# Kernel optimization log

Measured on AMD Instinct MI355X. Metric: run time of the kernel, lower is better.

## Reference

```python
import jax, jax.numpy as jnp
import numpy as np

N = 50000      # nodes
E = 800000     # edges (avg degree 16)
D = 128        # in_dim
H = 128        # hidden_dim
C = 10         # num_classes
G = 128        # graphs in batch
NUM_LAYERS = 3


def setup_inputs() -> dict:
    key = jax.random.key(0)
    ks = jax.random.split(key, 32)
    inp = {
        'features': jax.random.normal(ks[0], (N, D), dtype=jnp.float32),
        'src': jax.random.randint(ks[1], (E,), 0, N, dtype=jnp.int32),
        'dst': jax.random.randint(ks[2], (E,), 0, N, dtype=jnp.int32),
        'graph_ids': jnp.sort(jax.random.randint(ks[3], (N,), 0, G, dtype=jnp.int32)),
        'eps': jnp.zeros((NUM_LAYERS,), dtype=jnp.float32),  # learn_eps=True, init 0
    }
    # GIN MLPs: layer i has linear1 [in,H], linear2 [H,H] (stored as [in,out])
    ki = 4
    for i in range(NUM_LAYERS):
        din = D if i == 0 else H
        inp[f'w1_{i}'] = jax.random.normal(ks[ki], (din, H), dtype=jnp.float32) * (1.0 / np.sqrt(din)); ki += 1
        inp[f'b1_{i}'] = jnp.zeros((H,), dtype=jnp.float32)
        inp[f'w2_{i}'] = jax.random.normal(ks[ki], (H, H), dtype=jnp.float32) * (1.0 / np.sqrt(H)); ki += 1
        inp[f'b2_{i}'] = jnp.zeros((H,), dtype=jnp.float32)
    inp['wc1'] = jax.random.normal(ks[ki], (H, H), dtype=jnp.float32) * (1.0 / np.sqrt(H)); ki += 1
    inp['bc1'] = jnp.zeros((H,), dtype=jnp.float32)
    inp['wc2'] = jax.random.normal(ks[ki], (H, C), dtype=jnp.float32) * (1.0 / np.sqrt(H)); ki += 1
    inp['bc2'] = jnp.zeros((C,), dtype=jnp.float32)
    return inp


def _mlp(x, w1, b1, w2, b2):
    return jax.nn.relu(x @ w1 + b1) @ w2 + b2


def reference(features, src, dst, graph_ids, eps,
              w1_0, b1_0, w2_0, b2_0,
              w1_1, b1_1, w2_1, b2_1,
              w1_2, b1_2, w2_2, b2_2,
              wc1, bc1, wc2, bc2):
    mlps = [(w1_0, b1_0, w2_0, b2_0), (w1_1, b1_1, w2_1, b2_1), (w1_2, b1_2, w2_2, b2_2)]
    h = features
    for i, (w1, b1, w2, b2) in enumerate(mlps):
        # GINConv: aggregate sum of in-neighbor features (gather src, segment-sum into dst)
        agg = jax.ops.segment_sum(h[src], dst, num_segments=N)
        h = (1.0 + eps[i]) * h + agg
        h = _mlp(h, w1, b1, w2, b2)
        h = jax.nn.relu(h)
    # SumPooling: nodes -> graphs
    hg = jax.ops.segment_sum(h, graph_ids, num_segments=G)  # [G, H]
    out = jax.nn.relu(hg @ wc1 + bc1) @ wc2 + bc2            # [G, C]
    return out
```

## Files before the change

### kernel.cpp

```cpp
#include <hip/hip_runtime.h>

#define NN 50000
#define EE 800000
#define HH 128
#define CC 10
#define GG 128
#define NBK 782
#define NCH 98
#define CHUNK 8192

typedef __attribute__((ext_vector_type(8))) short short8;
typedef __attribute__((ext_vector_type(4))) float f32x4;

__device__ __forceinline__ ushort f2b(float f) {
    union { float f; uint u; } x; x.f = f;
    uint u = x.u;
    uint r = (u + 0x7fffu + ((u >> 16) & 1u)) >> 16;
    return (ushort)r;
}
__device__ __forceinline__ float lo2f(uint v) {
    union { uint u; float f; } x; x.u = v << 16; return x.f;
}
__device__ __forceinline__ float hi2f(uint v) {
    union { uint u; float f; } x; x.u = v & 0xffff0000u; return x.f;
}


__global__ __launch_bounds__(256) void hist_kernel(const int* __restrict__ dst,
                                                   int* __restrict__ hist) {
    __shared__ int hc[NBK];
    const int c = blockIdx.x, t = threadIdx.x;
    for (int k = t; k < NBK; k += 256) hc[k] = 0;
    __syncthreads();
    for (int j = 0; j < 32; ++j) {
        int e = c * CHUNK + j * 256 + t;
        if (e < EE) atomicAdd(&hc[dst[e] >> 6], 1);
    }
    __syncthreads();
    for (int k = t; k < NBK; k += 256) hist[k * NCH + c] = hc[k];
}

__global__ __launch_bounds__(128) void bscan_kernel(const int* __restrict__ hist,
                                                    int* __restrict__ rel,
                                                    int* __restrict__ btot) {
    __shared__ int s[128];
    const int b = blockIdx.x, t = threadIdx.x;
    int v = (t < NCH) ? hist[b * NCH + t] : 0;
    s[t] = v;
    __syncthreads();
    for (int off = 1; off < 128; off <<= 1) {
        int tt = (t >= off) ? s[t - off] : 0;
        __syncthreads();
        s[t] += tt;
        __syncthreads();
    }
    if (t < NCH) rel[b * NCH + t] = s[t] - v;
    if (t == 127) btot[b] = s[127];
}

__global__ __launch_bounds__(1024) void tscan_kernel(const int* __restrict__ btot,
                                                     int* __restrict__ bucketptr,
                                                     int* __restrict__ rowptr) {
    __shared__ int s[1024];
    const int t = threadIdx.x;
    int v = (t < NBK) ? btot[t] : 0;
    s[t] = v;
    __syncthreads();
    for (int off = 1; off < 1024; off <<= 1) {
        int tt = (t >= off) ? s[t - off] : 0;
        __syncthreads();
        s[t] += tt;
        __syncthreads();
    }
    if (t < NBK) bucketptr[t] = s[t] - v;
    if (t == 0) { bucketptr[NBK] = EE; rowptr[NN] = EE; }
}

__global__ __launch_bounds__(256) void scatter_kernel(const int* __restrict__ src,
                                                      const int* __restrict__ dst,
                                                      const int* __restrict__ rel,
                                                      const int* __restrict__ bucketptr,
                                                      int* __restrict__ epk) {
    __shared__ int cur[NBK];
    const int c = blockIdx.x, t = threadIdx.x;
    for (int k = t; k < NBK; k += 256) cur[k] = bucketptr[k] + rel[k * NCH + c];
    __syncthreads();
    for (int j = 0; j < 32; ++j) {
        int e = c * CHUNK + j * 256 + t;
        if (e < EE) {
            int d = dst[e];
            int bk = d >> 6;
            int pos = atomicAdd(&cur[bk], 1);
            epk[pos] = ((d & 63) << 16) | src[e];
        }
    }
}

__global__ __launch_bounds__(256) void bsort_kernel(const int* __restrict__ epk,
                                                    const int* __restrict__ bucketptr,
                                                    int* __restrict__ eidx,
                                                    int* __restrict__ rowptr) {
    __shared__ int cnt[64];
    __shared__ int cur[64];
    const int b = blockIdx.x, t = threadIdx.x;
    const int base = bucketptr[b], end = bucketptr[b + 1];
    if (t < 64) cnt[t] = 0;
    __syncthreads();
    for (int i = base + t; i < end; i += 256)
        atomicAdd(&cnt[(epk[i] >> 16) & 63], 1);
    __syncthreads();
    if (t < 64) {
        int v = cnt[t];
        int incl = v;
#pragma unroll
        for (int off = 1; off < 64; off <<= 1) {
            int u = __shfl_up(incl, off);
            if (t >= off) incl += u;
        }
        int excl = incl - v;
        cur[t] = excl;
        int node = b * 64 + t;
        if (node < NN) rowptr[node] = base + excl;
    }
    __syncthreads();
    for (int i = base + t; i < end; i += 256) {
        int p = epk[i];
        int dl = (p >> 16) & 63;
        int pos = atomicAdd(&cur[dl], 1);
        eidx[base + pos] = p & 0xffff;
    }
}


__global__ __launch_bounds__(256) void f2b_kernel(const float* __restrict__ in,
                                                  ushort* __restrict__ out, int n4) {
    int i = blockIdx.x * 256 + threadIdx.x;
    if (i < n4) {
        float4 v = ((const float4*)in)[i];
        ushort4 o;
        o.x = f2b(v.x); o.y = f2b(v.y); o.z = f2b(v.z); o.w = f2b(v.w);
        ((ushort4*)out)[i] = o;
    }
}

__global__ __launch_bounds__(256) void wconv_kernel(const float* w0, const float* w1,
                                                    const float* w2, const float* w3,
                                                    const float* w4, const float* w5,
                                                    ushort* __restrict__ wt) {
    const float* src;
    switch (blockIdx.y) {
        case 0: src = w0; break; case 1: src = w1; break;
        case 2: src = w2; break; case 3: src = w3; break;
        case 4: src = w4; break; default: src = w5; break;
    }
    int idx = blockIdx.x * 256 + threadIdx.x;
    int n = idx >> 7, k = idx & 127;
    wt[blockIdx.y * 16384 + n * 128 + k] = f2b(src[k * 128 + n]);
}


__global__ __launch_bounds__(256) void aggregate_kernel(const ushort* __restrict__ h,
                                                        const int* __restrict__ rowptr,
                                                        const int* __restrict__ eidx,
                                                        ushort* __restrict__ agg) {
    int node = blockIdx.x * 4 + (threadIdx.x >> 6);
    if (node >= NN) return;
    int lane = threadIdx.x & 63;
    int beg = rowptr[node], end = rowptr[node + 1];
    float ax = 0.f, ay = 0.f;
    int i = beg;
    for (; i + 8 <= end; i += 8) {
        uint v[8];
#pragma unroll
        for (int k = 0; k < 8; ++k) {
            int s = eidx[i + k];
            v[k] = *(const uint*)(h + (size_t)s * HH + lane * 2);
        }
#pragma unroll
        for (int k = 0; k < 8; ++k) { ax += lo2f(v[k]); ay += hi2f(v[k]); }
    }
    for (; i < end; ++i) {
        int s = eidx[i];
        uint v = *(const uint*)(h + (size_t)s * HH + lane * 2);
        ax += lo2f(v); ay += hi2f(v);
    }
    uint o = (uint)f2b(ax) | (((uint)f2b(ay)) << 16);
    *(uint*)(agg + (size_t)node * HH + lane * 2) = o;
}


__device__ __forceinline__ uint comb2(uint hv, uint av, float e) {
    float fl = e * lo2f(hv) + lo2f(av);
    float fh = e * hi2f(hv) + hi2f(av);
    return (uint)f2b(fl) | (((uint)f2b(fh)) << 16);
}

__global__ __launch_bounds__(256) void fused_mlp(const ushort* __restrict__ xin,
                                                 const ushort* __restrict__ agg,
                                                 const ushort* __restrict__ wt1,
                                                 const ushort* __restrict__ wt2,
                                                 const float* __restrict__ b1,
                                                 const float* __restrict__ b2,
                                                 const float* __restrict__ epsp, int layer,
                                                 ushort* __restrict__ out, int nrows) {
    __shared__ __align__(16) ushort xs[64][136];
    __shared__ __align__(16) ushort hs[64][136];
    const int tid = threadIdx.x;
    const int lane = tid & 63, w = tid >> 6;
    const int row0 = blockIdx.x * 64;
    const int l15 = lane & 15, lhi = lane >> 4;

    short8 a1[2][4], a2[2][4];
#pragma unroll
    for (int fa = 0; fa < 2; ++fa)
#pragma unroll
        for (int kt = 0; kt < 4; ++kt) {
            int n = w * 32 + fa * 16 + l15;
            int k = kt * 32 + lhi * 8;
            a1[fa][kt] = *(const short8*)(wt1 + n * HH + k);
            a2[fa][kt] = *(const short8*)(wt2 + n * HH + k);
        }

    float eps1 = 1.0f + epsp[layer];
#pragma unroll
    for (int it = 0; it < 4; ++it) {
        int idx = it * 256 + tid;
        int r = idx >> 4, kq = idx & 15;
        int row = row0 + r;
        uint4 xv = make_uint4(0u, 0u, 0u, 0u);
        if (row < nrows) {
            xv = *(const uint4*)(xin + (size_t)row * HH + kq * 8);
            uint4 av = *(const uint4*)(agg + (size_t)row * HH + kq * 8);
            xv.x = comb2(xv.x, av.x, eps1);
            xv.y = comb2(xv.y, av.y, eps1);
            xv.z = comb2(xv.z, av.z, eps1);
            xv.w = comb2(xv.w, av.w, eps1);
        }
        *(uint4*)&xs[r][kq * 8] = xv;
    }
    __syncthreads();

    f32x4 acc[2][4];
#pragma unroll
    for (int fa = 0; fa < 2; ++fa)
#pragma unroll
        for (int fb = 0; fb < 4; ++fb) acc[fa][fb] = (f32x4)(0.f);
#pragma unroll
    for (int kt = 0; kt < 4; ++kt) {
        short8 bfr[4];
#pragma unroll
        for (int fb = 0; fb < 4; ++fb)
            bfr[fb] = *(const short8*)&xs[fb * 16 + l15][kt * 32 + lhi * 8];
#pragma unroll
        for (int fa = 0; fa < 2; ++fa)
#pragma unroll
            for (int fb = 0; fb < 4; ++fb)
                acc[fa][fb] = __builtin_amdgcn_mfma_f32_16x16x32_bf16(a1[fa][kt], bfr[fb],
                                                                     acc[fa][fb], 0, 0, 0);
    }

#pragma unroll
    for (int fa = 0; fa < 2; ++fa) {
        int nb = w * 32 + fa * 16 + lhi * 4;
        float4 bv = *(const float4*)(b1 + nb);
#pragma unroll
        for (int fb = 0; fb < 4; ++fb) {
            ushort4 o;
            o.x = f2b(fmaxf(acc[fa][fb][0] + bv.x, 0.f));
            o.y = f2b(fmaxf(acc[fa][fb][1] + bv.y, 0.f));
            o.z = f2b(fmaxf(acc[fa][fb][2] + bv.z, 0.f));
            o.w = f2b(fmaxf(acc[fa][fb][3] + bv.w, 0.f));
            *(ushort4*)&hs[fb * 16 + l15][nb] = o;
        }
    }
    __syncthreads();

#pragma unroll
    for (int fa = 0; fa < 2; ++fa)
#pragma unroll
        for (int fb = 0; fb < 4; ++fb) acc[fa][fb] = (f32x4)(0.f);
#pragma unroll
    for (int kt = 0; kt < 4; ++kt) {
        short8 bfr[4];
#pragma unroll
        for (int fb = 0; fb < 4; ++fb)
            bfr[fb] = *(const short8*)&hs[fb * 16 + l15][kt * 32 + lhi * 8];
#pragma unroll
        for (int fa = 0; fa < 2; ++fa)
#pragma unroll
            for (int fb = 0; fb < 4; ++fb)
                acc[fa][fb] = __builtin_amdgcn_mfma_f32_16x16x32_bf16(a2[fa][kt], bfr[fb],
                                                                     acc[fa][fb], 0, 0, 0);
    }

#pragma unroll
    for (int fa = 0; fa < 2; ++fa) {
        int nb = w * 32 + fa * 16 + lhi * 4;
        float4 bv = *(const float4*)(b2 + nb);
#pragma unroll
        for (int fb = 0; fb < 4; ++fb) {
            int m = row0 + fb * 16 + l15;
            if (m < nrows) {
                ushort4 o;
                o.x = f2b(fmaxf(acc[fa][fb][0] + bv.x, 0.f));
                o.y = f2b(fmaxf(acc[fa][fb][1] + bv.y, 0.f));
                o.z = f2b(fmaxf(acc[fa][fb][2] + bv.z, 0.f));
                o.w = f2b(fmaxf(acc[fa][fb][3] + bv.w, 0.f));
                *(ushort4*)(out + (size_t)m * HH + nb) = o;
            }
        }
    }
}


__global__ __launch_bounds__(256) void pool_kernel(const ushort* __restrict__ h,
                                                   const int* __restrict__ gid,
                                                   float* hg) {
    int j = threadIdx.x & 63;
    int r0 = threadIdx.x >> 6;
    int n0 = blockIdx.x * 64;
    float ax = 0.f, ay = 0.f;
    int gcur = -1;
#pragma unroll
    for (int i = 0; i < 16; ++i) {
        int n = n0 + r0 + i * 4;
        if (n >= NN) break;
        int g = gid[n];
        if (g != gcur) {
            if (gcur >= 0) {
                atomicAdd(&hg[gcur * HH + 2 * j], ax);
                atomicAdd(&hg[gcur * HH + 2 * j + 1], ay);
            }
            gcur = g; ax = 0.f; ay = 0.f;
        }
        uint v = *(const uint*)(h + (size_t)n * HH + 2 * j);
        ax += lo2f(v); ay += hi2f(v);
    }
    if (gcur >= 0) {
        atomicAdd(&hg[gcur * HH + 2 * j], ax);
        atomicAdd(&hg[gcur * HH + 2 * j + 1], ay);
    }
}


__global__ __launch_bounds__(128) void classify_kernel(const float* __restrict__ hg,
                                                       const float* __restrict__ wc1,
                                                       const float* __restrict__ bc1,
                                                       const float* __restrict__ wc2,
                                                       const float* __restrict__ bc2,
                                                       float* __restrict__ out) {
    __shared__ float xrow[HH];
    __shared__ float trow[HH];
    int g = blockIdx.x, j = threadIdx.x;
    xrow[j] = hg[g * HH + j];
    __syncthreads();
    float s = bc1[j];
#pragma unroll 8
    for (int k = 0; k < HH; ++k) s += xrow[k] * wc1[k * HH + j];
    trow[j] = fmaxf(s, 0.f);
    __syncthreads();
    if (j < CC) {
        float o = bc2[j];
#pragma unroll 8
        for (int k = 0; k < HH; ++k) o += trow[k] * wc2[k * CC + j];
        out[g * CC + j] = o;
    }
}

extern "C" void kernel_launch(void* const* d_in, const int* in_sizes, int n_in,
                              void* d_out, int out_size, void* d_ws, size_t ws_size,
                              hipStream_t stream) {
    const float* features = (const float*)d_in[0];
    const int* src = (const int*)d_in[1];
    const int* dst = (const int*)d_in[2];
    const int* gid = (const int*)d_in[3];
    const float* eps = (const float*)d_in[4];
    const float* w1[3] = {(const float*)d_in[5], (const float*)d_in[9], (const float*)d_in[13]};
    const float* b1[3] = {(const float*)d_in[6], (const float*)d_in[10], (const float*)d_in[14]};
    const float* w2[3] = {(const float*)d_in[7], (const float*)d_in[11], (const float*)d_in[15]};
    const float* b2[3] = {(const float*)d_in[8], (const float*)d_in[12], (const float*)d_in[16]};
    const float* wc1 = (const float*)d_in[17];
    const float* bc1 = (const float*)d_in[18];
    const float* wc2 = (const float*)d_in[19];
    const float* bc2 = (const float*)d_in[20];
    float* outp = (float*)d_out;

    char* ws = (char*)d_ws;
    size_t off = 0;
    auto alloc = [&](size_t bytes) {
        void* p = ws + off;
        off += (bytes + 255) & ~(size_t)255;
        return p;
    };
    int* hist = (int*)alloc((size_t)NBK * NCH * sizeof(int));
    int* rel = (int*)alloc((size_t)NBK * NCH * sizeof(int));
    int* btot = (int*)alloc(NBK * sizeof(int));
    int* bucketptr = (int*)alloc((NBK + 1) * sizeof(int));
    int* epk = (int*)alloc(EE * sizeof(int));
    int* eidx = (int*)alloc(EE * sizeof(int));
    int* rowptr = (int*)alloc((NN + 1) * sizeof(int));
    ushort* hb0 = (ushort*)alloc((size_t)NN * HH * 2);
    ushort* hb1 = (ushort*)alloc((size_t)NN * HH * 2);
    ushort* hb2 = (ushort*)alloc((size_t)NN * HH * 2);
    ushort* aggb = (ushort*)alloc((size_t)NN * HH * 2);
    ushort* wtb = (ushort*)alloc(6 * 16384 * 2);
    float* hg = (float*)alloc(GG * HH * sizeof(float));

    hist_kernel<<<NCH, 256, 0, stream>>>(dst, hist);
    bscan_kernel<<<NBK, 128, 0, stream>>>(hist, rel, btot);
    tscan_kernel<<<1, 1024, 0, stream>>>(btot, bucketptr, rowptr);
    scatter_kernel<<<NCH, 256, 0, stream>>>(src, dst, rel, bucketptr, epk);
    bsort_kernel<<<NBK, 256, 0, stream>>>(epk, bucketptr, eidx, rowptr);

    f2b_kernel<<<(NN * HH / 4 + 255) / 256, 256, 0, stream>>>(features, hb0, NN * HH / 4);
    dim3 wg(64, 6);
    wconv_kernel<<<wg, 256, 0, stream>>>(w1[0], w2[0], w1[1], w2[1], w1[2], w2[2], wtb);

    const int GB = (NN + 63) / 64;

    const ushort* hin = hb0;
    ushort* houts[3] = {hb1, hb2, hb1};
    for (int i = 0; i < 3; ++i) {
        aggregate_kernel<<<(NN + 3) / 4, 256, 0, stream>>>(hin, rowptr, eidx, aggb);
        fused_mlp<<<GB, 256, 0, stream>>>(hin, aggb, wtb + (2 * i) * 16384,
                                          wtb + (2 * i + 1) * 16384,
                                          b1[i], b2[i], eps, i, houts[i], NN);
        hin = houts[i];
    }

    hipMemsetAsync(hg, 0, GG * HH * sizeof(float), stream);
    pool_kernel<<<(NN + 63) / 64, 256, 0, stream>>>(hb1, gid, hg);
    classify_kernel<<<GG, 128, 0, stream>>>(hg, wc1, bc1, wc2, bc2, outp);
}
```

Measured before the change: 246.8 us.

## Fuse eps-combine into aggregation, pooling into last MLP, split-edge gather

The aggregation kernel now has each wave split into two half-waves that process alternating edges with 8-byte loads, reduces the halves with a lane shuffle, and writes (1+eps)*h + agg directly. The MLP therefore reads one input tensor instead of two. The final layer's MLP writes its output into shared memory and does the graph sum-pooling with atomics, so the last hidden tensor is never written to global memory and the separate pool kernel is removed. The risks are lower memory-level parallelism per lane in the gather, and extra sync and atomic work added to the tail of the last MLP.

After: 233.3 us. 5.5% less time.

```diff
diff --git a/kernel.cpp b/kernel.cpp
--- a/kernel.cpp
+++ b/kernel.cpp
@@ -162,46 +162,58 @@
 __global__ __launch_bounds__(256) void aggregate_kernel(const ushort* __restrict__ h,
                                                         const int* __restrict__ rowptr,
                                                         const int* __restrict__ eidx,
-                                                        ushort* __restrict__ agg) {
+                                                        const float* __restrict__ epsp,
+                                                        int layer,
+                                                        ushort* __restrict__ xb) {
     int node = blockIdx.x * 4 + (threadIdx.x >> 6);
     if (node >= NN) return;
     int lane = threadIdx.x & 63;
+    int half = lane >> 5, li = lane & 31;
     int beg = rowptr[node], end = rowptr[node + 1];
-    float ax = 0.f, ay = 0.f;
-    int i = beg;
-    for (; i + 8 <= end; i += 8) {
-        uint v[8];
-#pragma unroll
-        for (int k = 0; k < 8; ++k) {
-            int s = eidx[i + k];
-            v[k] = *(const uint*)(h + (size_t)s * HH + lane * 2);
-        }
-#pragma unroll
-        for (int k = 0; k < 8; ++k) { ax += lo2f(v[k]); ay += hi2f(v[k]); }
-    }
-    for (; i < end; ++i) {
-        int s = eidx[i];
-        uint v = *(const uint*)(h + (size_t)s * HH + lane * 2);
-        ax += lo2f(v); ay += hi2f(v);
-    }
-    uint o = (uint)f2b(ax) | (((uint)f2b(ay)) << 16);
-    *(uint*)(agg + (size_t)node * HH + lane * 2) = o;
-}
-
-
-__device__ __forceinline__ uint comb2(uint hv, uint av, float e) {
-    float fl = e * lo2f(hv) + lo2f(av);
-    float fh = e * hi2f(hv) + hi2f(av);
-    return (uint)f2b(fl) | (((uint)f2b(fh)) << 16);
-}
-
-__global__ __launch_bounds__(256) void fused_mlp(const ushort* __restrict__ xin,
-                                                 const ushort* __restrict__ agg,
+    float c0 = 0.f, c1 = 0.f, c2 = 0.f, c3 = 0.f;
+    int i = beg + half;
+    for (; i + 6 < end; i += 8) {
+        int s0 = eidx[i], s1 = eidx[i + 2], s2 = eidx[i + 4], s3 = eidx[i + 6];
+        uint2 v0 = *(const uint2*)(h + (size_t)s0 * HH + li * 4);
+        uint2 v1 = *(const uint2*)(h + (size_t)s1 * HH + li * 4);
+        uint2 v2 = *(const uint2*)(h + (size_t)s2 * HH + li * 4);
+        uint2 v3 = *(const uint2*)(h + (size_t)s3 * HH + li * 4);
+        c0 += lo2f(v0.x) + lo2f(v1.x) + lo2f(v2.x) + lo2f(v3.x);
+        c1 += hi2f(v0.x) + hi2f(v1.x) + hi2f(v2.x) + hi2f(v3.x);
+        c2 += lo2f(v0.y) + lo2f(v1.y) + lo2f(v2.y) + lo2f(v3.y);
+        c3 += hi2f(v0.y) + hi2f(v1.y) + hi2f(v2.y) + hi2f(v3.y);
+    }
+    for (; i < end; i += 2) {
+        int s0 = eidx[i];
+        uint2 v0 = *(const uint2*)(h + (size_t)s0 * HH + li * 4);
+        c0 += lo2f(v0.x); c1 += hi2f(v0.x);
+        c2 += lo2f(v0.y); c3 += hi2f(v0.y);
+    }
+    c0 += __shfl_xor(c0, 32);
+    c1 += __shfl_xor(c1, 32);
+    c2 += __shfl_xor(c2, 32);
+    c3 += __shfl_xor(c3, 32);
+    if (half == 0) {
+        uint2 hv = *(const uint2*)(h + (size_t)node * HH + li * 4);
+        float e = 1.0f + epsp[layer];
+        ushort4 o;
+        o.x = f2b(e * lo2f(hv.x) + c0);
+        o.y = f2b(e * hi2f(hv.x) + c1);
+        o.z = f2b(e * lo2f(hv.y) + c2);
+        o.w = f2b(e * hi2f(hv.y) + c3);
+        *(ushort4*)(xb + (size_t)node * HH + li * 4) = o;
+    }
+}
+
+
+template <bool LAST>
+__global__ __launch_bounds__(256) void fused_mlp(const ushort* __restrict__ xb,
                                                  const ushort* __restrict__ wt1,
                                                  const ushort* __restrict__ wt2,
                                                  const float* __restrict__ b1,
                                                  const float* __restrict__ b2,
-                                                 const float* __restrict__ epsp, int layer,
+                                                 const int* __restrict__ gid,
+                                                 float* __restrict__ hg,
                                                  ushort* __restrict__ out, int nrows) {
     __shared__ __align__(16) ushort xs[64][136];
     __shared__ __align__(16) ushort hs[64][136];
@@ -221,21 +233,13 @@
             a2[fa][kt] = *(const short8*)(wt2 + n * HH + k);
         }
 
-    float eps1 = 1.0f + epsp[layer];
 #pragma unroll
     for (int it = 0; it < 4; ++it) {
         int idx = it * 256 + tid;
         int r = idx >> 4, kq = idx & 15;
         int row = row0 + r;
         uint4 xv = make_uint4(0u, 0u, 0u, 0u);
-        if (row < nrows) {
-            xv = *(const uint4*)(xin + (size_t)row * HH + kq * 8);
-            uint4 av = *(const uint4*)(agg + (size_t)row * HH + kq * 8);
-            xv.x = comb2(xv.x, av.x, eps1);
-            xv.y = comb2(xv.y, av.y, eps1);
-            xv.z = comb2(xv.z, av.z, eps1);
-            xv.w = comb2(xv.w, av.w, eps1);
-        }
+        if (row < nrows) xv = *(const uint4*)(xb + (size_t)row * HH + kq * 8);
         *(uint4*)&xs[r][kq * 8] = xv;
     }
     __syncthreads();
@@ -300,45 +304,45 @@
 #pragma unroll
         for (int fb = 0; fb < 4; ++fb) {
             int m = row0 + fb * 16 + l15;
-            if (m < nrows) {
-                ushort4 o;
-                o.x = f2b(fmaxf(acc[fa][fb][0] + bv.x, 0.f));
-                o.y = f2b(fmaxf(acc[fa][fb][1] + bv.y, 0.f));
-                o.z = f2b(fmaxf(acc[fa][fb][2] + bv.z, 0.f));
-                o.w = f2b(fmaxf(acc[fa][fb][3] + bv.w, 0.f));
+            ushort4 o;
+            o.x = f2b(fmaxf(acc[fa][fb][0] + bv.x, 0.f));
+            o.y = f2b(fmaxf(acc[fa][fb][1] + bv.y, 0.f));
+            o.z = f2b(fmaxf(acc[fa][fb][2] + bv.z, 0.f));
+            o.w = f2b(fmaxf(acc[fa][fb][3] + bv.w, 0.f));
+            if (LAST) {
+                *(ushort4*)&xs[fb * 16 + l15][nb] = o;
+            } else if (m < nrows) {
                 *(ushort4*)(out + (size_t)m * HH + nb) = o;
             }
         }
     }
-}
-
-
-__global__ __launch_bounds__(256) void pool_kernel(const ushort* __restrict__ h,
-                                                   const int* __restrict__ gid,
-                                                   float* hg) {
-    int j = threadIdx.x & 63;
-    int r0 = threadIdx.x >> 6;
-    int n0 = blockIdx.x * 64;
-    float ax = 0.f, ay = 0.f;
-    int gcur = -1;
-#pragma unroll
-    for (int i = 0; i < 16; ++i) {
-        int n = n0 + r0 + i * 4;
-        if (n >= NN) break;
-        int g = gid[n];
-        if (g != gcur) {
-            if (gcur >= 0) {
-                atomicAdd(&hg[gcur * HH + 2 * j], ax);
-                atomicAdd(&hg[gcur * HH + 2 * j + 1], ay);
+
+    if (LAST) {
+        __syncthreads();
+        int j = tid & 63;
+        int rg = tid >> 6;
+        float ax = 0.f, ay = 0.f;
+        int gcur = -1;
+#pragma unroll
+        for (int ii = 0; ii < 16; ++ii) {
+            int r = rg + ii * 4;
+            int n = row0 + r;
+            if (n >= nrows) break;
+            int g = gid[n];
+            if (g != gcur) {
+                if (gcur >= 0) {
+                    atomicAdd(&hg[gcur * HH + 2 * j], ax);
+                    atomicAdd(&hg[gcur * HH + 2 * j + 1], ay);
+                }
+                gcur = g; ax = 0.f; ay = 0.f;
             }
-            gcur = g; ax = 0.f; ay = 0.f;
-        }
-        uint v = *(const uint*)(h + (size_t)n * HH + 2 * j);
-        ax += lo2f(v); ay += hi2f(v);
-    }
-    if (gcur >= 0) {
-        atomicAdd(&hg[gcur * HH + 2 * j], ax);
-        atomicAdd(&hg[gcur * HH + 2 * j + 1], ay);
+            uint v = *(const uint*)&xs[r][2 * j];
+            ax += lo2f(v); ay += hi2f(v);
+        }
+        if (gcur >= 0) {
+            atomicAdd(&hg[gcur * HH + 2 * j], ax);
+            atomicAdd(&hg[gcur * HH + 2 * j + 1], ay);
+        }
     }
 }
 
@@ -400,9 +404,8 @@
     int* eidx = (int*)alloc(EE * sizeof(int));
     int* rowptr = (int*)alloc((NN + 1) * sizeof(int));
     ushort* hb0 = (ushort*)alloc((size_t)NN * HH * 2);
-    ushort* hb1 = (ushort*)alloc((size_t)NN * HH * 2);
-    ushort* hb2 = (ushort*)alloc((size_t)NN * HH * 2);
-    ushort* aggb = (ushort*)alloc((size_t)NN * HH * 2);
+    ushort* hbuf = (ushort*)alloc((size_t)NN * HH * 2);
+    ushort* xb = (ushort*)alloc((size_t)NN * HH * 2);
     ushort* wtb = (ushort*)alloc(6 * 16384 * 2);
     float* hg = (float*)alloc(GG * HH * sizeof(float));
 
@@ -416,19 +419,20 @@
     dim3 wg(64, 6);
     wconv_kernel<<<wg, 256, 0, stream>>>(w1[0], w2[0], w1[1], w2[1], w1[2], w2[2], wtb);
 
+    hipMemsetAsync(hg, 0, GG * HH * sizeof(float), stream);
+
     const int GB = (NN + 63) / 64;
-
-    const ushort* hin = hb0;
-    ushort* houts[3] = {hb1, hb2, hb1};
-    for (int i = 0; i < 3; ++i) {
-        aggregate_kernel<<<(NN + 3) / 4, 256, 0, stream>>>(hin, rowptr, eidx, aggb);
-        fused_mlp<<<GB, 256, 0, stream>>>(hin, aggb, wtb + (2 * i) * 16384,
-                                          wtb + (2 * i + 1) * 16384,
-                                          b1[i], b2[i], eps, i, houts[i], NN);
-        hin = houts[i];
-    }
-
-    hipMemsetAsync(hg, 0, GG * HH * sizeof(float), stream);
-    pool_kernel<<<(NN + 63) / 64, 256, 0, stream>>>(hb1, gid, hg);
+    const int AB = (NN + 3) / 4;
+
+    aggregate_kernel<<<AB, 256, 0, stream>>>(hb0, rowptr, eidx, eps, 0, xb);
+    fused_mlp<false><<<GB, 256, 0, stream>>>(xb, wtb + 0 * 16384, wtb + 1 * 16384,
+                                             b1[0], b2[0], gid, hg, hbuf, NN);
+    aggregate_kernel<<<AB, 256, 0, stream>>>(hbuf, rowptr, eidx, eps, 1, xb);
+    fused_mlp<false><<<GB, 256, 0, stream>>>(xb, wtb + 2 * 16384, wtb + 3 * 16384,
+                                             b1[1], b2[1], gid, hg, hbuf, NN);
+    aggregate_kernel<<<AB, 256, 0, stream>>>(hbuf, rowptr, eidx, eps, 2, xb);
+    fused_mlp<true><<<GB, 256, 0, stream>>>(xb, wtb + 4 * 16384, wtb + 5 * 16384,
+                                            b1[2], b2[2], gid, hg, nullptr, NN);
+
     classify_kernel<<<GG, 128, 0, stream>>>(hg, wc1, bc1, wc2, bc2, outp);
 }
```
